# Kernel tuning notes

Measured on AMD Instinct MI355X. Metric: run time of the kernel, lower is better.

The kernel has to match this reference:

```python
import jax, jax.numpy as jnp
import numpy as np

CM = 8        # channel_mult
EPS = 1e-5    # BatchNorm eps
NEG = 0.2     # LeakyReLU slope


def conv2d(x, w, stride, pad, b=None):
    y = jax.lax.conv_general_dilated(
        x, w, (stride, stride), [(pad, pad), (pad, pad)],
        dimension_numbers=('NCHW', 'OIHW', 'NCHW'))
    if b is not None:
        y = y + b[None, :, None, None]
    return y


def per_sample_conv(x, w, stride, pad):
    # x: [B,C,H,W], w: [B,O,C,kh,kw] -> per-sample conv, vmapped over batch
    f = lambda xi, wi: conv2d(xi[None], wi, stride, pad)[0]
    return jax.vmap(f)(x, w)


def batchnorm(x, g, b):
    # training-mode BN: batch statistics over (N,H,W)
    m = jnp.mean(x, axis=(0, 2, 3), keepdims=True)
    v = jnp.var(x, axis=(0, 2, 3), keepdims=True)
    return (x - m) * jax.lax.rsqrt(v + EPS) * g[None, :, None, None] + b[None, :, None, None]


def lrelu(x):
    return jnp.where(x >= 0, x, NEG * x)


def setup_inputs() -> dict:
    key = jax.random.key(0)
    ks = jax.random.split(key, 16)
    B, H, W = 16, 512, 512

    def rn(k, shape, fan_in):
        return jax.random.normal(k, shape, jnp.float32) * np.float32(1.0 / np.sqrt(fan_in))

    inp = {}
    inp['x'] = jax.random.normal(ks[0], (B, 3, H, W), jnp.float32)
    n_meta = 3 * (CM // 2) * 25 + CM * (CM * 2 // 2) * 25  # 300 + 1600 = 1900
    inp['conv_weights'] = jax.random.normal(ks[1], (B, n_meta), jnp.float32) * 0.05
    inp['w11'] = rn(ks[2], (CM // 2, 3, 5, 5), 3 * 25)
    inp['b11'] = jnp.zeros((CM // 2,), jnp.float32)
    inp['w12'] = rn(ks[3], (CM * 2 // 2, CM, 5, 5), CM * 25)
    inp['b12'] = jnp.zeros((CM * 2 // 2,), jnp.float32)
    inp['bn1_g'] = jnp.ones((CM * 2,), jnp.float32)
    inp['bn1_b'] = jnp.zeros((CM * 2,), jnp.float32)
    # conv2 stack: (in, out, kernel)
    chans = [(CM * 2, CM * 4, 5), (CM * 4, CM * 8, 5), (CM * 8, CM * 16, 3), (CM * 16, CM * 16, 3)]
    for i, (ci, co, k) in enumerate(chans, 1):
        inp[f'c2w{i}'] = rn(ks[3 + i], (co, ci, k, k), ci * k * k)
        inp[f'c2b{i}'] = jnp.zeros((co,), jnp.float32)
        inp[f'bn{i}g'] = jnp.ones((co,), jnp.float32)
        inp[f'bn{i}b'] = jnp.zeros((co,), jnp.float32)
    return inp


def reference(x, conv_weights, w11, b11, w12, b12, bn1_g, bn1_b,
              c2w1, c2b1, bn1g, bn1b, c2w2, c2b2, bn2g, bn2b,
              c2w3, c2b3, bn3g, bn3b, c2w4, c2b4, bn4g, bn4b):
    B, _, H, W = x.shape
    n1 = 3 * (CM // 2) * 25
    w1 = conv_weights[:, :n1].reshape(B, CM // 2, 3, 5, 5)
    w2 = conv_weights[:, n1:].reshape(B, CM * 2 // 2, CM, 5, 5)

    # meta layer 1: shared half + per-sample dynamic half
    xx = conv2d(x, w11, 1, 2, b11)                  # [B, cm/2, H, W]
    half = per_sample_conv(x, w1, 1, 2)             # [B, cm/2, H, W]
    h = lrelu(jnp.concatenate([xx, half], axis=1))  # [B, cm, H, W]

    # meta layer 2 (stride 2)
    xx = conv2d(h, w12, 2, 2, b12)                  # [B, cm, H/2, W/2]
    half = per_sample_conv(h, w2, 2, 2)             # [B, cm, H/2, W/2]
    h = lrelu(batchnorm(jnp.concatenate([xx, half], axis=1), bn1_g, bn1_b))

    # dense conv stack
    for w_, b_, g_, be_, p in [
        (c2w1, c2b1, bn1g, bn1b, 2),
        (c2w2, c2b2, bn2g, bn2b, 2),
        (c2w3, c2b3, bn3g, bn3b, 1),
        (c2w4, c2b4, bn4g, bn4b, 1),
    ]:
        h = lrelu(batchnorm(conv2d(h, w_, 2, p, b_), g_, be_))

    return h.reshape(-1, CM * 16, H // 32, W // 32)
```

## Files before the change

kernel.cpp:

```cpp
#include <hip/hip_runtime.h>


typedef __attribute__((ext_vector_type(8))) short short8v;
typedef __attribute__((ext_vector_type(4))) float float4v;
typedef __attribute__((ext_vector_type(4))) unsigned short ushort4v;
typedef unsigned short u16;

#define LRELU_NEG 0.2f
#define BN_EPS 1e-5f

__device__ __forceinline__ float bf2f(u16 u){ union{unsigned i; float f;} v; v.i=(unsigned)u<<16; return v.f; }
__device__ __forceinline__ u16 f2bf(float f){ unsigned x=__float_as_uint(f); x += 0x7FFFu + ((x>>16)&1u); return (u16)(x>>16); }
__device__ __forceinline__ float lrelu(float v){ return v<0.f? LRELU_NEG*v : v; }

__device__ __forceinline__ void packw(int i, const float* __restrict__ w, u16* __restrict__ dst,
                                      int IC, int OC, int KSZ, int CPR) {
  int kq = i & 31, oc = (i>>5) % OC, c = i/(OC*32);
  int ky = c / CPR, r = c % CPR;
  int kk = r*32 + kq; int kx = kk / IC, ic = kk % IC;
  float v = (kx < KSZ) ? w[(((size_t)oc*IC + ic)*KSZ + ky)*KSZ + kx] : 0.f;
  dst[i] = f2bf(v);
}

__global__ __launch_bounds__(256) void prep_all(
    const float* __restrict__ w11, const float* __restrict__ w12,
    const float* __restrict__ b12, const float* __restrict__ cw,
    const float* __restrict__ wc1, const float* __restrict__ wc2,
    const float* __restrict__ wc3, const float* __restrict__ wc4,
    u16* __restrict__ wl1d, u16* __restrict__ wl2m, float* __restrict__ bl2,
    u16* __restrict__ d1, u16* __restrict__ d2, u16* __restrict__ d3, u16* __restrict__ d4,
    u16* __restrict__ h1) {
  int i = blockIdx.x*256 + threadIdx.x;
  if (i < 16) {
    bl2[i] = (i<8)? b12[i] : 0.f;
  } else if (i < 49168) {
    int j = i - 16;
    int b = j / 3072, r = j % 3072;
    int c = r >> 9, r2 = r & 511;
    int row = r2 >> 5, kk = r2 & 31;
    int kx = kk >> 2, ic = kk & 3;
    int grp = row >> 3, oc = row & 7;
    int ky = c - grp;
    float v = 0.f;
    if (ic < 3 && kx < 5 && ky >= 0 && ky < 5)
      v = (oc < 4) ? w11[((oc*3+ic)*5+ky)*5+kx]
                   : cw[b*1900 + (oc-4)*75 + ic*25 + ky*5 + kx];
    wl1d[j] = f2bf(v);
  } else if (i < 131088) {
    int j = i - 49168;
    int kq = j & 31, oc = (j>>5) & 15, c = (j>>9) % 10, b = j / 5120;
    int ky = c >> 1, r = c & 1;
    int kk = r*32 + kq; int kx = kk >> 3, ic = kk & 7;
    float v = 0.f;
    if (kx < 5)
      v = (oc < 8) ? w12[((oc*8+ic)*5+ky)*5+kx]
                   : cw[b*1900 + 300 + ((oc-8)*8+ic)*25 + ky*5 + kx];
    wl2m[j] = f2bf(v);
  } else if (i < 196880) {
    int j = i - 131088;
    int b = j / 4112, p = j % 4112;
    int y, xx;
    if (p < 2064) { int r = p/516; y = (r<2)? r : 512+r; xx = p%516; }
    else          { int q = p-2064; int cidx = q&3; xx = (cidx<2)? cidx : 512+cidx; y = 2 + (q>>2); }
    short8v z = {0,0,0,0,0,0,0,0};
    *(short8v*)(h1 + (((size_t)b*516 + y)*516 + xx)*8) = z;
  } else if (i < 484624) {
    int j = i - 196880;
    if (j < 15360) packw(j, wc1, d1, 16, 32, 5, 3);
    else if (j < 66560) packw(j-15360, wc2, d2, 32, 64, 5, 5);
    else if (j < 140288) packw(j-66560, wc3, d3, 64, 128, 3, 6);
    else packw(j-140288, wc4, d4, 128, 128, 3, 12);
  }
}

__global__ __launch_bounds__(256) void conv_l1(const float* __restrict__ x,
    const u16* __restrict__ wl1d, const float* __restrict__ b11,
    u16* __restrict__ h1) {
  __shared__ u16 sx[12*72*4];
  const int tid = threadIdx.x, b = blockIdx.z;
  const int x0 = (blockIdx.x & 7) * 64;
  const int r0 = (blockIdx.x >> 3) * 8;

  const bool interior = (r0 >= 2) & (r0 <= 502) & (x0 >= 2) & (x0 <= 442);
  if (interior) {
    for (int e = tid; e < 864; e += 256) {
      int row = e / 72, col = e % 72;
      size_t base = ((size_t)b*3*512 + r0 + row - 2)*512 + x0 + col - 2;
      ushort4 pk = {f2bf(x[base]), f2bf(x[base + 262144]), f2bf(x[base + 524288]), 0};
      *(ushort4*)(sx + e*4) = pk;
    }
  } else {
    for (int e = tid; e < 864; e += 256) {
      int row = e / 72, col = e % 72;
      int gy = r0 + row - 2, gx = x0 + col - 2;
      float v0 = 0.f, v1 = 0.f, v2 = 0.f;
      if (gy >= 0 && gy < 512 && gx >= 0 && gx < 512) {
        size_t base = ((size_t)b*3*512 + gy)*512 + gx;
        v0 = x[base]; v1 = x[base + 262144]; v2 = x[base + 524288];
      }
      ushort4 pk = {f2bf(v0), f2bf(v1), f2bf(v2), 0};
      *(ushort4*)(sx + e*4) = pk;
    }
  }
  __syncthreads();

  const int lane = tid & 63, w = tid >> 6;
  const int l15 = lane & 15, sub = lane >> 4;

  short8v Wf[6];
  const u16* wb = wl1d + (size_t)b*3072;
#pragma unroll
  for (int c = 0; c < 6; c++)
    Wf[c] = *(const short8v*)(wb + (c*16 + l15)*32 + sub*8);

  float bvv[4];
#pragma unroll
  for (int r = 0; r < 4; r++) bvv[r] = (sub & 1) ? 0.f : b11[r];

  const int colb = w*16 + l15;
  const int oc0 = (sub & 1) * 4;
  const int rsel = sub >> 1;

#pragma unroll
  for (int p = 0; p < 4; p++) {
    float4v acc = {0.f, 0.f, 0.f, 0.f};
#pragma unroll
    for (int c = 0; c < 6; c++) {
      const u16* ap = sx + (((2*p + c)*72 + colb) << 2) + sub*8;
      union { unsigned long long q[2]; short8v v; } ua;
      ua.q[0] = *(const unsigned long long*)(ap);
      ua.q[1] = *(const unsigned long long*)(ap + 4);
      acc = __builtin_amdgcn_mfma_f32_16x16x32_bf16(Wf[c], ua.v, acc, 0, 0, 0);
    }
    ushort4v pk;
#pragma unroll
    for (int r = 0; r < 4; r++) pk[r] = f2bf(lrelu(acc[r] + bvv[r]));
    int outrow = r0 + 2*p + rsel;
    u16* dst = h1 + (((size_t)b*516 + outrow + 2)*516 + x0 + colb + 2)*8 + oc0;
    *(ushort4v*)dst = pk;
  }
}

template <int IC, int OC, int KSZ, int S, int P, int CPR, int NCH,
          int IPH, int IPW, int OWL, int OPH, int OPW,
          int WM, int WN, int WVM, int WVN, bool PERS>
__global__ __launch_bounds__(WVM*WVN*64) void conv_mfma(
    const u16* __restrict__ in, const u16* __restrict__ wmfma,
    const float* __restrict__ bias, u16* __restrict__ out,
    float2* __restrict__ part2) {
  constexpr int OW = 1 << OWL;
  constexpr int PADOFF = 2 - P;
  const int tid = threadIdx.x, lane = tid & 63;
  const int w = tid >> 6, wm = w % WVM, wn = w / WVM;
  const int l15 = lane & 15, sub = lane >> 4;
  const int b = blockIdx.z;
  const int px0 = blockIdx.x * (16*WM*WVM) + wm * (16*WM);
  const int oc0 = blockIdx.y * (16*WN*WVN) + wn * (16*WN);

  int oyf[WM], oxb[WM], ixb[WM];
#pragma unroll
  for (int f = 0; f < WM; f++) {
    int p = px0 + f*16;
    oyf[f] = p >> OWL;
    oxb[f] = p & (OW-1);
    ixb[f] = S*(oxb[f] + l15) + PADOFF;
  }
  const u16* inb = in + (size_t)b*IPH*IPW*IC;
  const u16* wbase = wmfma + (PERS ? (size_t)b*NCH*OC*32 : (size_t)0);

  float4v acc[WM][WN];
#pragma unroll
  for (int f = 0; f < WM; f++)
#pragma unroll
    for (int n = 0; n < WN; n++) acc[f][n] = (float4v){0.f,0.f,0.f,0.f};

#pragma unroll
  for (int ky = 0; ky < KSZ; ky++) {
#pragma unroll
    for (int r = 0; r < CPR; r++) {
      const int c = ky*CPR + r;
      const int kk0 = r*32 + sub*8;
      const int kx = kk0 / IC;
      const int icoff = kk0 % IC;
      short8v B[WN];
#pragma unroll
      for (int n = 0; n < WN; n++)
        B[n] = *(const short8v*)(wbase + ((size_t)c*OC + oc0 + n*16 + l15)*32 + sub*8);
      short8v A[WM];
#pragma unroll
      for (int f = 0; f < WM; f++) {
        int iy = S*oyf[f] + ky + PADOFF;
        A[f] = *(const short8v*)(inb + ((size_t)iy*IPW + ixb[f] + kx)*IC + icoff);
      }
#pragma unroll
      for (int f = 0; f < WM; f++)
#pragma unroll
        for (int n = 0; n < WN; n++)
          acc[f][n] = __builtin_amdgcn_mfma_f32_16x16x32_bf16(A[f], B[n], acc[f][n], 0, 0, 0);
    }
  }

  float s[WN], q[WN];
#pragma unroll
  for (int n = 0; n < WN; n++) { s[n] = 0.f; q[n] = 0.f; }
#pragma unroll
  for (int f = 0; f < WM; f++) {
    const int oxs = oxb[f] + sub*4;
    const size_t rowb = ((size_t)b*OPH + oyf[f] + 2)*OPW;
#pragma unroll
    for (int n = 0; n < WN; n++) {
      int oc = oc0 + n*16 + l15;
      float bv = bias[oc];
#pragma unroll
      for (int rr = 0; rr < 4; rr++) {
        float v = acc[f][n][rr] + bv;
        out[(rowb + oxs + rr + 2)*OC + oc] = f2bf(v);
        s[n] += v; q[n] += v*v;
      }
    }
  }
#pragma unroll
  for (int n = 0; n < WN; n++) {
    s[n] += __shfl_xor(s[n], 16); s[n] += __shfl_xor(s[n], 32);
    q[n] += __shfl_xor(q[n], 16); q[n] += __shfl_xor(q[n], 32);
  }
  __shared__ float sred[WVM*WVN][WN][16][2];
  if (sub == 0) {
#pragma unroll
    for (int n = 0; n < WN; n++) { sred[w][n][l15][0] = s[n]; sred[w][n][l15][1] = q[n]; }
  }
  __syncthreads();
  const int NBp = gridDim.x * gridDim.z;
  const int pb = blockIdx.z * gridDim.x + blockIdx.x;
  const int tot = WVN*WN*16;
  if (tid < tot) {
    int c16 = tid & 15, n = (tid >> 4) % WN, wn2 = tid / (16*WN);
    float S_ = 0.f, Q_ = 0.f;
    for (int wm2 = 0; wm2 < WVM; wm2++) {
      S_ += sred[wn2*WVM + wm2][n][c16][0];
      Q_ += sred[wn2*WVM + wm2][n][c16][1];
    }
    int c = blockIdx.y*(16*WN*WVN) + wn2*(16*WN) + n*16 + c16;
    part2[(size_t)c*NBp + pb] = make_float2(S_, Q_);
  }
}

__global__ void bn_stage2(const float2* __restrict__ part2, const float* __restrict__ g,
                          const float* __restrict__ bb, float* __restrict__ stats,
                          int NBp, float invN) {
  int c = blockIdx.x;
  float s = 0.f, q = 0.f;
  for (int i = threadIdx.x; i < NBp; i += 64) {
    float2 p = part2[(size_t)c*NBp + i];
    s += p.x; q += p.y;
  }
  for (int o = 32; o > 0; o >>= 1) { s += __shfl_down(s, o); q += __shfl_down(q, o); }
  if (threadIdx.x == 0) {
    float m = s * invN;
    float var = q * invN - m*m;
    float sc = g[c] * rsqrtf(var + BN_EPS);
    stats[2*c] = sc;
    stats[2*c+1] = bb[c] - m*sc;
  }
}

template <int C, int PH, int PW, int HH, int WW>
__global__ __launch_bounds__(256) void bn_fin(u16* __restrict__ y, const float* __restrict__ stats,
                                              int total8) {
  int i = blockIdx.x*256 + threadIdx.x;
  if (i >= total8) return;
  size_t e = (size_t)i*8;
  int c0 = (int)(e & (C-1));
  int px = (int)(e / C);
  int xx = px % PW;
  int yy = (px / PW) % PH;
  bool interior = (yy >= 2) & (yy < 2+HH) & (xx >= 2) & (xx < 2+WW);
  short8v u = *(short8v*)(y + e);
  short8v o;
#pragma unroll
  for (int j = 0; j < 8; j++) {
    float v = bf2f((u16)u[j]) * stats[2*(c0+j)] + stats[2*(c0+j)+1];
    o[j] = interior ? (short)f2bf(lrelu(v)) : (short)0;
  }
  *(short8v*)(y + e) = o;
}

__global__ __launch_bounds__(256) void out_k(const u16* __restrict__ y6,
                                             const float* __restrict__ stats,
                                             float* __restrict__ out) {
  int i = blockIdx.x*256 + threadIdx.x;
  if (i >= 131072) return;
  size_t e = (size_t)i*4;
  int c0 = (int)(e & 127);
  int px = (int)(e >> 7);
  int loc = px & 255, b = px >> 8;
  int y = loc >> 4, x = loc & 15;
  const u16* src = y6 + (((size_t)b*20 + y + 2)*20 + x + 2)*128 + c0;
  ushort4 u = *(const ushort4*)src;
  float vv[4] = {bf2f(u.x), bf2f(u.y), bf2f(u.z), bf2f(u.w)};
#pragma unroll
  for (int j = 0; j < 4; j++) {
    int c = c0 + j;
    float v = vv[j] * stats[2*c] + stats[2*c+1];
    out[(((size_t)b*128 + c) << 8) + loc] = lrelu(v);
  }
}

extern "C" void kernel_launch(void* const* d_in, const int* in_sizes, int n_in,
                              void* d_out, int out_size, void* d_ws, size_t ws_size,
                              hipStream_t stream) {
  const float* x    = (const float*)d_in[0];
  const float* cw   = (const float*)d_in[1];
  const float* w11  = (const float*)d_in[2];
  const float* b11  = (const float*)d_in[3];
  const float* w12  = (const float*)d_in[4];
  const float* b12  = (const float*)d_in[5];
  const float* bn1g = (const float*)d_in[6];
  const float* bn1b = (const float*)d_in[7];
  const float* c2w[4] = {(const float*)d_in[8], (const float*)d_in[12],
                         (const float*)d_in[16], (const float*)d_in[20]};
  const float* c2b[4] = {(const float*)d_in[9], (const float*)d_in[13],
                         (const float*)d_in[17], (const float*)d_in[21]};
  const float* bng[4] = {(const float*)d_in[10], (const float*)d_in[14],
                         (const float*)d_in[18], (const float*)d_in[22]};
  const float* bnb[4] = {(const float*)d_in[11], (const float*)d_in[15],
                         (const float*)d_in[19], (const float*)d_in[23]};

  char* ws = (char*)d_ws;
  u16* h1   = (u16*)(ws);
  u16* y3   = (u16*)(ws);
  u16* y4   = (u16*)(ws + 17842176);
  u16* y5   = (u16*)(ws + 27312128);
  u16* y6   = (u16*)(ws + 32620544);
  u16* yT2  = (u16*)(ws + 68158464);
  u16* wl2m = (u16*)(ws + 102769664);
  float* bl2    = (float*)(ws + 102933504);
  float2* part2 = (float2*)(ws + 102933568);
  float* stats2 = (float*)(ws + 103457856);
  float* stats3 = stats2 + 32;
  float* stats4 = stats3 + 64;
  float* stats5 = stats4 + 128;
  float* stats6 = stats5 + 256;
  u16* wl1d = (u16*)(ws + 103460800);
  u16* wS1  = (u16*)(ws + 103559104);
  u16* wS2  = (u16*)(ws + 103589824);
  u16* wS3  = (u16*)(ws + 103692224);
  u16* wS4  = (u16*)(ws + 103839680);

  prep_all<<<1894, 256, 0, stream>>>(w11, w12, b12, cw,
                                     c2w[0], c2w[1], c2w[2], c2w[3],
                                     wl1d, wl2m, bl2, wS1, wS2, wS3, wS4, h1);

  conv_l1<<<dim3(512, 1, 16), 256, 0, stream>>>(x, wl1d, b11, h1);

  conv_mfma<8,16,5,2,2, 2,10, 516,516, 8, 260,260, 4,1,4,1, true>
      <<<dim3(256,1,16), 256, 0, stream>>>(h1, wl2m, bl2, yT2, part2);

  bn_stage2<<<16, 64, 0, stream>>>(part2, bn1g, bn1b, stats2, 4096, 1.f/1048576.f);
  bn_fin<16,260,260,256,256><<<8450, 256, 0, stream>>>(yT2, stats2, 2163200);

  conv_mfma<16,32,5,2,2, 3,15, 260,260, 7, 132,132, 2,2,4,1, false>
      <<<dim3(128,1,16), 256, 0, stream>>>(yT2, wS1, c2b[0], y3, part2);
  bn_stage2<<<32, 64, 0, stream>>>(part2, bng[0], bnb[0], stats3, 2048, 1.f/262144.f);
  bn_fin<32,132,132,128,128><<<4356, 256, 0, stream>>>(y3, stats3, 1115136);

  conv_mfma<32,64,5,2,2, 5,25, 132,132, 6, 68,68, 2,2,2,2, false>
      <<<dim3(64,1,16), 256, 0, stream>>>(y3, wS2, c2b[1], y4, part2);
  bn_stage2<<<64, 64, 0, stream>>>(part2, bng[1], bnb[1], stats4, 1024, 1.f/65536.f);
  bn_fin<64,68,68,64,64><<<2312, 256, 0, stream>>>(y4, stats4, 591872);

  conv_mfma<64,128,3,2,1, 6,18, 68,68, 5, 36,36, 2,2,2,2, false>
      <<<dim3(16,2,16), 256, 0, stream>>>(y4, wS3, c2b[2], y5, part2);
  bn_stage2<<<128, 64, 0, stream>>>(part2, bng[2], bnb[2], stats5, 256, 1.f/16384.f);
  bn_fin<128,36,36,32,32><<<1296, 256, 0, stream>>>(y5, stats5, 331776);

  conv_mfma<128,128,3,2,1, 12,36, 36,36, 4, 20,20, 2,2,1,2, false>
      <<<dim3(8,2,16), 128, 0, stream>>>(y5, wS4, c2b[3], y6, part2);
  bn_stage2<<<128, 64, 0, stream>>>(part2, bng[3], bnb[3], stats6, 128, 1.f/4096.f);

  out_k<<<512, 256, 0, stream>>>(y6, stats6, (float*)d_out);
}
```

Baseline: 271.7 us.

## Enlarge conv_l1 tiles with vectorized loads and double-buffer conv_mfma operand loads

conv_l1 now processes 16 output rows per block instead of 8, halving the grid, and loads the interior input tile with float4 vector loads, packing to bf16 in shared memory with a shifted column offset. conv_mfma replaces its single-buffered load-then-MFMA loop with a two-stage ping-pong. The next chunk's A/B fragments are loaded while the current chunk's MFMAs issue, hiding global load latency. This costs more registers per thread and fewer blocks for layer 1, which may reduce occupancy.

New measurement: 268.2 us. No clear change (-1.3%).

```diff
diff --git a/kernel.cpp b/kernel.cpp
--- a/kernel.cpp
+++ b/kernel.cpp
@@ -76,23 +76,37 @@
 __global__ __launch_bounds__(256) void conv_l1(const float* __restrict__ x,
     const u16* __restrict__ wl1d, const float* __restrict__ b11,
     u16* __restrict__ h1) {
-  __shared__ u16 sx[12*72*4];
+  __shared__ __align__(16) u16 sx[20*72*4 + 32];
   const int tid = threadIdx.x, b = blockIdx.z;
   const int x0 = (blockIdx.x & 7) * 64;
-  const int r0 = (blockIdx.x >> 3) * 8;
-
-  const bool interior = (r0 >= 2) & (r0 <= 502) & (x0 >= 2) & (x0 <= 442);
+  const int r0 = (blockIdx.x >> 3) * 16;
+
+  if (tid < 32) sx[20*72*4 + tid] = 0;
+
+  const bool interior = (r0 >= 16) & (r0 <= 480) & (x0 >= 64) & (x0 <= 384);
   if (interior) {
-    for (int e = tid; e < 864; e += 256) {
+    for (int e = tid; e < 360; e += 256) {
+      int row = e / 18, cg = e % 18;
+      size_t base = ((size_t)b*3*512 + r0 + row - 2)*512 + x0 + cg*4 - 4;
+      float4v p0 = *(const float4v*)(x + base);
+      float4v p1 = *(const float4v*)(x + base + 262144);
+      float4v p2 = *(const float4v*)(x + base + 524288);
+      short8v lo, hi;
+#pragma unroll
+      for (int j = 0; j < 2; j++) {
+        lo[4*j+0] = (short)f2bf(p0[j]);   lo[4*j+1] = (short)f2bf(p1[j]);
+        lo[4*j+2] = (short)f2bf(p2[j]);   lo[4*j+3] = 0;
+        hi[4*j+0] = (short)f2bf(p0[j+2]); hi[4*j+1] = (short)f2bf(p1[j+2]);
+        hi[4*j+2] = (short)f2bf(p2[j+2]); hi[4*j+3] = 0;
+      }
+      u16* dp = sx + (row*72 + cg*4)*4;
+      *(short8v*)dp = lo;
+      *(short8v*)(dp + 8) = hi;
+    }
+  } else {
+    for (int e = tid; e < 1440; e += 256) {
       int row = e / 72, col = e % 72;
-      size_t base = ((size_t)b*3*512 + r0 + row - 2)*512 + x0 + col - 2;
-      ushort4 pk = {f2bf(x[base]), f2bf(x[base + 262144]), f2bf(x[base + 524288]), 0};
-      *(ushort4*)(sx + e*4) = pk;
-    }
-  } else {
-    for (int e = tid; e < 864; e += 256) {
-      int row = e / 72, col = e % 72;
-      int gy = r0 + row - 2, gx = x0 + col - 2;
+      int gy = r0 + row - 2, gx = x0 + col - 4;
       float v0 = 0.f, v1 = 0.f, v2 = 0.f;
       if (gy >= 0 && gy < 512 && gx >= 0 && gx < 512) {
         size_t base = ((size_t)b*3*512 + gy)*512 + gx;
@@ -122,11 +136,11 @@
   const int rsel = sub >> 1;
 
 #pragma unroll
-  for (int p = 0; p < 4; p++) {
+  for (int p = 0; p < 8; p++) {
     float4v acc = {0.f, 0.f, 0.f, 0.f};
 #pragma unroll
     for (int c = 0; c < 6; c++) {
-      const u16* ap = sx + (((2*p + c)*72 + colb) << 2) + sub*8;
+      const u16* ap = sx + (((2*p + c)*72 + colb + 2) << 2) + sub*8;
       union { unsigned long long q[2]; short8v v; } ua;
       ua.q[0] = *(const unsigned long long*)(ap);
       ua.q[1] = *(const unsigned long long*)(ap + 4);
@@ -140,6 +154,24 @@
     *(ushort4v*)dst = pk;
   }
 }
+
+#define LOADC(cc, Ax, Bx) do {                                                   \
+    const int ky_ = (cc) / CPR, r_ = (cc) % CPR;                                 \
+    const int kk0_ = r_*32 + sub*8;                                              \
+    const int kx_ = kk0_ / IC, ico_ = kk0_ % IC;                                 \
+    _Pragma("unroll") for (int n_ = 0; n_ < WN; n_++)                            \
+      Bx[n_] = *(const short8v*)(wbase + ((size_t)(cc)*OC + oc0 + n_*16 + l15)*32 + sub*8); \
+    _Pragma("unroll") for (int f_ = 0; f_ < WM; f_++) {                          \
+      int iy_ = S*oyf[f_] + ky_ + PADOFF;                                        \
+      Ax[f_] = *(const short8v*)(inb + ((size_t)iy_*IPW + ixb[f_] + kx_)*IC + ico_); \
+    }                                                                            \
+  } while(0)
+
+#define MFMAC(Ax, Bx) do {                                                       \
+    _Pragma("unroll") for (int f_ = 0; f_ < WM; f_++)                            \
+      _Pragma("unroll") for (int n_ = 0; n_ < WN; n_++)                          \
+        acc[f_][n_] = __builtin_amdgcn_mfma_f32_16x16x32_bf16(Ax[f_], Bx[n_], acc[f_][n_], 0, 0, 0); \
+  } while(0)
 
 template <int IC, int OC, int KSZ, int S, int P, int CPR, int NCH,
           int IPH, int IPW, int OWL, int OPH, int OPW,
@@ -174,30 +206,15 @@
 #pragma unroll
     for (int n = 0; n < WN; n++) acc[f][n] = (float4v){0.f,0.f,0.f,0.f};
 
-#pragma unroll
-  for (int ky = 0; ky < KSZ; ky++) {
-#pragma unroll
-    for (int r = 0; r < CPR; r++) {
-      const int c = ky*CPR + r;
-      const int kk0 = r*32 + sub*8;
-      const int kx = kk0 / IC;
-      const int icoff = kk0 % IC;
-      short8v B[WN];
-#pragma unroll
-      for (int n = 0; n < WN; n++)
-        B[n] = *(const short8v*)(wbase + ((size_t)c*OC + oc0 + n*16 + l15)*32 + sub*8);
-      short8v A[WM];
-#pragma unroll
-      for (int f = 0; f < WM; f++) {
-        int iy = S*oyf[f] + ky + PADOFF;
-        A[f] = *(const short8v*)(inb + ((size_t)iy*IPW + ixb[f] + kx)*IC + icoff);
-      }
-#pragma unroll
-      for (int f = 0; f < WM; f++)
-#pragma unroll
-        for (int n = 0; n < WN; n++)
-          acc[f][n] = __builtin_amdgcn_mfma_f32_16x16x32_bf16(A[f], B[n], acc[f][n], 0, 0, 0);
-    }
+  constexpr int NC = KSZ * CPR;
+  short8v A0[WM], B0[WN], A1[WM], B1[WN];
+  LOADC(0, A0, B0);
+#pragma unroll
+  for (int c = 0; c < NC; c += 2) {
+    if (c + 1 < NC) LOADC(c + 1, A1, B1);
+    MFMAC(A0, B0);
+    if (c + 2 < NC) LOADC(c + 2, A0, B0);
+    if (c + 1 < NC) MFMAC(A1, B1);
   }
 
   float s[WN], q[WN];
@@ -351,7 +368,7 @@
                                      c2w[0], c2w[1], c2w[2], c2w[3],
                                      wl1d, wl2m, bl2, wS1, wS2, wS3, wS4, h1);
 
-  conv_l1<<<dim3(512, 1, 16), 256, 0, stream>>>(x, wl1d, b11, h1);
+  conv_l1<<<dim3(256, 1, 16), 256, 0, stream>>>(x, wl1d, b11, h1);
 
   conv_mfma<8,16,5,2,2, 2,10, 516,516, 8, 260,260, 4,1,4,1, true>
       <<<dim3(256,1,16), 256, 0, stream>>>(h1, wl2m, bl2, yT2, part2);
```
